# Kernel tuning notes

Hardware: AMD Instinct MI355X
Metric: run time of the kernel (lower is better)

The kernel has to match this reference:

```python
import jax, jax.numpy as jnp
import numpy as np

NUM_HEADS = 4
LOCAL_RADIUS = 2


def setup_inputs() -> dict:
    key = jax.random.key(0)
    ks = jax.random.split(key, 7)
    B, C, H, W = 1, 256, 40, 40
    O = 256  # out_channels
    s = 1.0 / np.sqrt(C).astype(np.float32)
    x = jax.random.normal(ks[0], (B, C, H, W), dtype=jnp.float32)
    Wq = jax.random.normal(ks[1], (C, O), dtype=jnp.float32) * s
    Wk = jax.random.normal(ks[2], (C, O), dtype=jnp.float32) * s
    Wv = jax.random.normal(ks[3], (C, O), dtype=jnp.float32) * s
    bq = jnp.zeros((O,), jnp.float32)
    bk = jnp.zeros((O,), jnp.float32)
    bv = jnp.zeros((O,), jnp.float32)
    return {"x": x, "Wq": Wq, "bq": bq, "Wk": Wk, "bk": bk, "Wv": Wv, "bv": bv}


def reference(x, Wq, bq, Wk, bk, Wv, bv):
    B, C, H, W = x.shape
    N = H * W
    O = Wq.shape[1]
    hd = O // NUM_HEADS
    # Faithful to torch: x.view(B, N, -1) is a raw row-major reshape of (B,C,H,W)
    xf = x.reshape(B, N, C)
    # projections -> (B, heads, N, head_dim)
    q = (xf @ Wq + bq).reshape(B, N, NUM_HEADS, hd).transpose(0, 2, 1, 3)
    k = (xf @ Wk + bk).reshape(B, N, NUM_HEADS, hd).transpose(0, 2, 1, 3)
    v = (xf @ Wv + bv).reshape(B, N, NUM_HEADS, hd).transpose(0, 2, 1, 3)
    scale = jnp.asarray(O, jnp.float32) ** 0.5
    acc = jnp.zeros_like(v)
    # 25 shifted full-attention passes; roll is over (heads, points) axes,
    # exactly matching torch key.roll(shifts=(h,w), dims=(-3,-2)).
    for h in range(-LOCAL_RADIUS, LOCAL_RADIUS + 1):
        for w in range(-LOCAL_RADIUS, LOCAL_RADIUS + 1):
            rk = jnp.roll(k, shift=(h, w), axis=(1, 2))
            scores = jnp.einsum('bhnd,bhmd->bhnm', q, rk) / scale  # (B,h,N,N)
            attn = jax.nn.softmax(scores, axis=-1)
            rv = jnp.roll(v, shift=(-h, -w), axis=(1, 2))
            acc = acc + jnp.einsum('bhnm,bhmd->bhnd', attn, rv)
    # (B, heads, N, hd) -> (B, N, O)
    return acc.transpose(0, 2, 1, 3).reshape(B, N, O)
```

## Files before the change

kernel.cpp:

```cpp
#include <hip/hip_runtime.h>
#include <hip/hip_bf16.h>
#include <stdint.h>

typedef __attribute__((ext_vector_type(8))) __bf16 bf16x8;
typedef __attribute__((ext_vector_type(4))) float f32x4;

#define N_PTS 1600
#define HD    64

#define OFF_XC   0u
#define OFF_WT   819200u
#define OFF_BIAS 1212416u
#define OFF_VHT  1213952u
#define OFF_QH   2033152u
#define OFF_KH   2852352u
#define OFF_KF   0u
#define OFF_OP   2852352u
#define OFF_LP   9405952u
#define OFF_VF   9610752u

__device__ __forceinline__ float bf2f(ushort h) {
  union { uint32_t u; float f; } v; v.u = ((uint32_t)h) << 16; return v.f;
}
__device__ __forceinline__ ushort f2bf(float f) {
  union { float f; uint32_t u; } v; v.f = f;
  uint32_t u = v.u;
  return (ushort)((u + 0x7FFFu + ((u >> 16) & 1u)) >> 16);
}
__device__ __forceinline__ uint32_t pk2(float a, float b) {
  union { __hip_bfloat162 h; uint32_t u; } cv;
  cv.h = __float22bfloat162_rn(make_float2(a, b));
  return cv.u;
}

__device__ __forceinline__ int detect_f32(const ushort* xu, int* shflag) {
  int t = threadIdx.x & 255;
  if (t == 0) *shflag = 0;
  __syncthreads();
  int local = 0;
#pragma unroll
  for (int i = 0; i < 4; ++i) {
    float v = bf2f(xu[(t * 4 + i) * 2]);
    if (!(fabsf(v) < 1e4f)) local = 1;
  }
  if (local) atomicOr(shflag, 1);
  __syncthreads();
  return *shflag;
}

__global__ void k_prep(const void* __restrict__ x, const void* __restrict__ Wq,
                       const void* __restrict__ bq, const void* __restrict__ Wk,
                       const void* __restrict__ bk, const void* __restrict__ Wv,
                       const void* __restrict__ bv, char* __restrict__ ws) {
  __shared__ int shflag;
  __shared__ ushort tileb[32][33];
  int isf32 = detect_f32((const ushort*)x, &shflag);
  int b = blockIdx.x, t = threadIdx.x;

  if (b < 400) {
    ushort4 o;
    if (isf32) {
      float4 f = ((const float4*)x)[b * 256 + t];
      o.x = f2bf(f.x); o.y = f2bf(f.y); o.z = f2bf(f.z); o.w = f2bf(f.w);
    } else {
      o = ((const ushort4*)x)[b * 256 + t];
    }
    ((ushort4*)(ws + OFF_XC))[b * 256 + t] = o;
  } else if (b < 592) {
    int w = b - 400, z = w >> 6, tile = w & 63;
    const void* W = (z == 0) ? Wq : ((z == 1) ? Wk : Wv);
    int o0 = (tile & 7) * 32, k0 = (tile >> 3) * 32;
    int tx = t & 31, ty = t >> 5;
#pragma unroll
    for (int i = 0; i < 32; i += 8) {
      int kk = (k0 + ty + i) * 256 + o0 + tx;
      tileb[ty + i][tx] = isf32 ? f2bf(((const float*)W)[kk]) : ((const ushort*)W)[kk];
    }
    __syncthreads();
    ushort* WT = (ushort*)(ws + OFF_WT) + z * 65536;
#pragma unroll
    for (int i = 0; i < 32; i += 8)
      WT[(o0 + ty + i) * 256 + k0 + tx] = tileb[tx][ty + i];
  } else {
    ushort* bb = (ushort*)(ws + OFF_BIAS);
#pragma unroll
    for (int z = 0; z < 3; ++z) {
      const void* B = (z == 0) ? bq : ((z == 1) ? bk : bv);
      bb[z * 256 + t] = isf32 ? f2bf(((const float*)B)[t]) : ((const ushort*)B)[t];
    }
  }
}

__launch_bounds__(256)
__global__ void k_proj(const ushort* __restrict__ X, const ushort* __restrict__ WT,
                       const ushort* __restrict__ bias3,
                       ushort* __restrict__ Qh, ushort* __restrict__ Kh, ushort* __restrict__ VhT) {
  int z = blockIdx.z;
  const ushort* WTz = WT + z * 65536;
  const ushort* bias = bias3 + z * 256;
  int n0 = blockIdx.x * 16;
  int head = threadIdx.x >> 6;
  int lane = threadIdx.x & 63;
  int c = lane & 15, quad = lane >> 4;

  f32x4 acc[4];
#pragma unroll
  for (int i = 0; i < 4; ++i) acc[i] = (f32x4){0.f, 0.f, 0.f, 0.f};

  const ushort* xrow = X + (n0 + c) * 256;
#pragma unroll
  for (int kt = 0; kt < 8; ++kt) {
    bf16x8 a = *(const bf16x8*)(xrow + kt * 32 + quad * 8);
#pragma unroll
    for (int os = 0; os < 4; ++os) {
      bf16x8 bfr = *(const bf16x8*)(WTz + (head * 64 + os * 16 + c) * 256 + kt * 32 + quad * 8);
      acc[os] = __builtin_amdgcn_mfma_f32_16x16x32_bf16(a, bfr, acc[os], 0, 0, 0);
    }
  }
  if (z == 2) {
#pragma unroll
    for (int os = 0; os < 4; ++os) {
      float bval = bf2f(bias[head * 64 + os * 16 + c]);
      ushort4 v;
      v.x = f2bf(acc[os][0] + bval); v.y = f2bf(acc[os][1] + bval);
      v.z = f2bf(acc[os][2] + bval); v.w = f2bf(acc[os][3] + bval);
      *(ushort4*)(VhT + (head * 64 + os * 16 + c) * N_PTS + n0 + quad * 4) = v;
    }
  } else {
    float scale = (z == 0) ? 0.0625f * 1.44269504088896f : 1.0f;
    ushort* out = (z == 0) ? Qh : Kh;
#pragma unroll
    for (int os = 0; os < 4; ++os) {
      float bval = bf2f(bias[head * 64 + os * 16 + c]);
#pragma unroll
      for (int r = 0; r < 4; ++r)
        out[head * (N_PTS * HD) + (n0 + quad * 4 + r) * HD + os * 16 + c] =
            f2bf((acc[os][r] + bval) * scale);
    }
  }
}

__global__ void k_frag(const ushort* __restrict__ Kh, const ushort* __restrict__ VhT,
                       ushort* __restrict__ Kf, ushort* __restrict__ Vf) {
  int q = blockIdx.x * 256 + threadIdx.x;
  int isV = q >= 51200;
  int idx = isV ? q - 51200 : q;
  int lane = idx & 63, ch = (idx >> 6) & 3;
  int rest = idx >> 8;
  int t = rest % 50, g = rest / 50;
  int c = lane & 15, quad = lane >> 4;
  if (!isV) {
    int perm = ((c >> 2) << 3) + (c & 3);
    int key = t * 32 + perm + ((ch >> 1) << 2);
    int d0 = (ch & 1) * 32 + quad * 8;
    bf16x8 v = *(const bf16x8*)(Kh + (size_t)(g * N_PTS + key) * HD + d0);
    *(bf16x8*)(Kf + (size_t)idx * 8) = v;
  } else {
    int d = ch * 16 + c;
    int m0 = t * 32 + quad * 8;
    const ushort* row = VhT + (size_t)(g * HD + d) * N_PTS;
    int mp = (m0 == 0) ? 1592 : m0 - 8;
    int mn = (m0 == 1592) ? 0 : m0 + 8;
    union { bf16x8 v[3]; ushort us[24]; } w;
    w.v[0] = *(const bf16x8*)(row + mp);
    w.v[1] = *(const bf16x8*)(row + m0);
    w.v[2] = *(const bf16x8*)(row + mn);
    union { ushort us[8]; bf16x8 v; } o;
#pragma unroll
    for (int j = 0; j < 8; ++j) {
      float s = bf2f(w.us[4 + j]) + bf2f(w.us[6 + j]) + bf2f(w.us[8 + j]) +
                bf2f(w.us[10 + j]) + bf2f(w.us[12 + j]);
      o.us[j] = f2bf(s);
    }
    *(bf16x8*)(Vf + (size_t)idx * 8) = o.v;
  }
}

__device__ __forceinline__ bf16x8 pack_p8(const f32x4& s0, const f32x4& s1, float& lp) {
  float e0 = exp2f(s0[0]), e1 = exp2f(s0[1]), e2 = exp2f(s0[2]), e3 = exp2f(s0[3]);
  float e4 = exp2f(s1[0]), e5 = exp2f(s1[1]), e6 = exp2f(s1[2]), e7 = exp2f(s1[3]);
  lp += ((e0 + e1) + (e2 + e3)) + ((e4 + e5) + (e6 + e7));
  union { uint32_t u[4]; bf16x8 v; } r;
  r.u[0] = pk2(e0, e1); r.u[1] = pk2(e2, e3);
  r.u[2] = pk2(e4, e5); r.u[3] = pk2(e6, e7);
  return r.v;
}

#define MFMA16(a, b, cc) __builtin_amdgcn_mfma_f32_16x16x32_bf16(a, b, cc, 0, 0, 0)

#define LOADT(sfx, t) do {                                            \
    const char* kt_ = kfp + (size_t)(t) * 4096;                       \
    const char* vt_ = vfp + (size_t)(t) * 4096;                       \
    ka0##sfx = *(const bf16x8*)(kt_);                                 \
    ka1##sfx = *(const bf16x8*)(kt_ + 1024);                          \
    kb0##sfx = *(const bf16x8*)(kt_ + 2048);                          \
    kb1##sfx = *(const bf16x8*)(kt_ + 3072);                          \
    vb0##sfx = *(const bf16x8*)(vt_);                                 \
    vb1##sfx = *(const bf16x8*)(vt_ + 1024);                          \
    vb2##sfx = *(const bf16x8*)(vt_ + 2048);                          \
    vb3##sfx = *(const bf16x8*)(vt_ + 3072);                          \
  } while (0)

#define COMPUTE(sfx) do {                                             \
    __builtin_amdgcn_s_setprio(1);                                    \
    f32x4 s0 = MFMA16(ka0##sfx, qa00, z4);                            \
    s0 = MFMA16(ka1##sfx, qa01, s0);                                  \
    f32x4 s1 = MFMA16(kb0##sfx, qa00, z4);                            \
    s1 = MFMA16(kb1##sfx, qa01, s1);                                  \
    bf16x8 pa0 = pack_p8(s0, s1, lp0);                                \
    oacc0[0] = MFMA16(pa0, vb0##sfx, oacc0[0]);                       \
    oacc0[1] = MFMA16(pa0, vb1##sfx, oacc0[1]);                       \
    oacc0[2] = MFMA16(pa0, vb2##sfx, oacc0[2]);                       \
    oacc0[3] = MFMA16(pa0, vb3##sfx, oacc0[3]);                       \
    s0 = MFMA16(ka0##sfx, qa10, z4);                                  \
    s0 = MFMA16(ka1##sfx, qa11, s0);                                  \
    s1 = MFMA16(kb0##sfx, qa10, z4);                                  \
    s1 = MFMA16(kb1##sfx, qa11, s1);                                  \
    bf16x8 pa1 = pack_p8(s0, s1, lp1);                                \
    oacc1[0] = MFMA16(pa1, vb0##sfx, oacc1[0]);                       \
    oacc1[1] = MFMA16(pa1, vb1##sfx, oacc1[1]);                       \
    oacc1[2] = MFMA16(pa1, vb2##sfx, oacc1[2]);                       \
    oacc1[3] = MFMA16(pa1, vb3##sfx, oacc1[3]);                       \
    __builtin_amdgcn_s_setprio(0);                                    \
  } while (0)

__launch_bounds__(256)
__global__ void k_attn(const ushort* __restrict__ Qh, const ushort* __restrict__ Kf,
                       const ushort* __restrict__ Vf, ushort* __restrict__ Opart,
                       float* __restrict__ Lpart) {
  int qt = blockIdx.x;
  int yy = blockIdx.y;
  int hp = yy >> 2, kg = yy & 3;
  int vg = (2 * hp - kg + 8) & 3;
  int tid = threadIdx.x, sp = tid >> 6, lane = tid & 63;
  int c = lane & 15, quad = lane >> 4;
  int n0 = qt * 16;

  __shared__ float obuf[4][16][68];
  __shared__ float lbuf[4][16];

  const ushort* q0row = Qh + ((hp    ) * N_PTS + n0 + c) * HD;
  const ushort* q1row = Qh + ((hp + 2) * N_PTS + n0 + c) * HD;
  bf16x8 qa00 = *(const bf16x8*)(q0row + quad * 8);
  bf16x8 qa01 = *(const bf16x8*)(q0row + 32 + quad * 8);
  bf16x8 qa10 = *(const bf16x8*)(q1row + quad * 8);
  bf16x8 qa11 = *(const bf16x8*)(q1row + 32 + quad * 8);

  f32x4 oacc0[4], oacc1[4];
#pragma unroll
  for (int i = 0; i < 4; ++i) {
    oacc0[i] = (f32x4){0.f, 0.f, 0.f, 0.f};
    oacc1[i] = (f32x4){0.f, 0.f, 0.f, 0.f};
  }
  float lp0 = 0.f, lp1 = 0.f;

  int off = (sp == 0) ? 0 : (sp == 1) ? 13 : (sp == 2) ? 26 : 38;
  int iters = (sp < 2) ? 13 : 12;
  const f32x4 z4 = (f32x4){0.f, 0.f, 0.f, 0.f};

  const char* kfp = (const char*)Kf + (size_t)(kg * 50 + off) * 4096 + lane * 16;
  const char* vfp = (const char*)Vf + (size_t)(vg * 50 + off) * 4096 + lane * 16;

  bf16x8 ka0A, ka1A, kb0A, kb1A, vb0A, vb1A, vb2A, vb3A;
  bf16x8 ka0B, ka1B, kb0B, kb1B, vb0B, vb1B, vb2B, vb3B;

  LOADT(A, 0);
  int it = 0;
  for (; it + 2 <= iters; it += 2) {
    LOADT(B, it + 1);
    COMPUTE(A);
    int tn = (it + 2 < iters) ? (it + 2) : (it + 1);
    LOADT(A, tn);
    COMPUTE(B);
  }
  if (it < iters) COMPUTE(A);

  lp0 += __shfl_xor(lp0, 16, 64); lp0 += __shfl_xor(lp0, 32, 64);
  lp1 += __shfl_xor(lp1, 16, 64); lp1 += __shfl_xor(lp1, 32, 64);

#pragma unroll
  for (int h = 0; h < 2; ++h) {
    __syncthreads();
    const f32x4* oa = h ? oacc1 : oacc0;
#pragma unroll
    for (int ds = 0; ds < 4; ++ds)
#pragma unroll
      for (int r = 0; r < 4; ++r)
        obuf[sp][quad * 4 + r][ds * 16 + c] = oa[ds][r];
    if (quad == 0) lbuf[sp][c] = h ? lp1 : lp0;
    __syncthreads();

    int q = tid >> 4, d0 = (tid & 15) * 4;
    f32x4 a = *(const f32x4*)&obuf[0][q][d0];
    a += *(const f32x4*)&obuf[1][q][d0];
    a += *(const f32x4*)&obuf[2][q][d0];
    a += *(const f32x4*)&obuf[3][q][d0];
    float l = lbuf[0][q] + lbuf[1][q] + lbuf[2][q] + lbuf[3][q];
    int hq = hp + 2 * h;
    union { uint32_t u[2]; } wv;
    wv.u[0] = pk2(a[0], a[1]);
    wv.u[1] = pk2(a[2], a[3]);
    *(uint2*)&Opart[(size_t)(kg * N_PTS + n0 + q) * 256 + hq * 64 + d0] =
        *(uint2*)wv.u;
    if ((tid & 15) == 0)
      Lpart[(kg * 4 + hq) * N_PTS + n0 + q] = l;
  }
}

__global__ void k_out(const ushort* __restrict__ Opart, const float* __restrict__ Lpart,
                      const void* __restrict__ x, void* __restrict__ out) {
  __shared__ int shflag;
  int isf32 = detect_f32((const ushort*)x, &shflag);
  int idx = blockIdx.x * 256 + threadIdx.x;
  int n = idx >> 8, o = idx & 255, hq = o >> 6;
  float acc = 0.f;
#pragma unroll
  for (int kg = 0; kg < 4; ++kg) {
    float num = bf2f(Opart[(size_t)(kg * N_PTS + n) * 256 + o]);
    float l = Lpart[(kg * 4 + hq) * N_PTS + n];
    float w = (kg == ((hq + 2) & 3)) ? 2.f : 1.f;
    acc += w * num / l;
  }
  if (isf32) ((float*)out)[idx] = acc;
  else       ((ushort*)out)[idx] = f2bf(acc);
}

extern "C" void kernel_launch(void* const* d_in, const int* in_sizes, int n_in,
                              void* d_out, int out_size, void* d_ws, size_t ws_size,
                              hipStream_t stream) {
  char* ws = (char*)d_ws;
  ushort* Xc    = (ushort*)(ws + OFF_XC);
  ushort* WT    = (ushort*)(ws + OFF_WT);
  ushort* bias3 = (ushort*)(ws + OFF_BIAS);
  ushort* VhT   = (ushort*)(ws + OFF_VHT);
  ushort* Qh    = (ushort*)(ws + OFF_QH);
  ushort* Kh    = (ushort*)(ws + OFF_KH);
  ushort* Kf    = (ushort*)(ws + OFF_KF);
  ushort* Vf    = (ushort*)(ws + OFF_VF);
  ushort* Opart = (ushort*)(ws + OFF_OP);
  float*  Lpart = (float*)(ws + OFF_LP);

  k_prep<<<593, 256, 0, stream>>>(d_in[0], d_in[1], d_in[2], d_in[3],
                                  d_in[4], d_in[5], d_in[6], ws);
  k_proj<<<dim3(100, 1, 3), 256, 0, stream>>>(Xc, WT, bias3, Qh, Kh, VhT);
  k_frag<<<400, 256, 0, stream>>>(Kh, VhT, Kf, Vf);
  k_attn<<<dim3(100, 8), 256, 0, stream>>>(Qh, Kf, Vf, Opart, Lpart);
  k_out<<<1600, 256, 0, stream>>>(Opart, Lpart, d_in[0], d_out);
}
```

Before: 116.6 us.

## Fuse x conversion into projection and output combine into attention kernel

Drops the separate x-to-bf16 staging pass from the prep kernel and converts fp32 x on the fly inside the projection kernel. Restructures the attention launch so each 512-thread block handles all four key groups for a head pair across eight waves, two per group, splitting the sequence in halves. The normalization and weighted combine are then done in shared memory and written straight to the output, which removes the separate output kernel and its partial-result round trip through global memory. In exchange there are fewer attention blocks (200 instead of 800), so fewer blocks are in flight, and each block uses more shared memory.

Result: faster. 109.4 us (-6.2%).

```diff
diff --git a/kernel.cpp b/kernel.cpp
--- a/kernel.cpp
+++ b/kernel.cpp
@@ -8,16 +8,13 @@
 #define N_PTS 1600
 #define HD    64
 
-#define OFF_XC   0u
-#define OFF_WT   819200u
-#define OFF_BIAS 1212416u
-#define OFF_VHT  1213952u
-#define OFF_QH   2033152u
-#define OFF_KH   2852352u
-#define OFF_KF   0u
-#define OFF_OP   2852352u
-#define OFF_LP   9405952u
-#define OFF_VF   9610752u
+#define OFF_WT   0u
+#define OFF_BIAS 393216u
+#define OFF_VHT  394752u
+#define OFF_QH   1213952u
+#define OFF_KH   2033152u
+#define OFF_KF   2852352u
+#define OFF_VF   3671552u
 
 __device__ __forceinline__ float bf2f(ushort h) {
   union { uint32_t u; float f; } v; v.u = ((uint32_t)h) << 16; return v.f;
@@ -57,17 +54,8 @@
   int isf32 = detect_f32((const ushort*)x, &shflag);
   int b = blockIdx.x, t = threadIdx.x;
 
-  if (b < 400) {
-    ushort4 o;
-    if (isf32) {
-      float4 f = ((const float4*)x)[b * 256 + t];
-      o.x = f2bf(f.x); o.y = f2bf(f.y); o.z = f2bf(f.z); o.w = f2bf(f.w);
-    } else {
-      o = ((const ushort4*)x)[b * 256 + t];
-    }
-    ((ushort4*)(ws + OFF_XC))[b * 256 + t] = o;
-  } else if (b < 592) {
-    int w = b - 400, z = w >> 6, tile = w & 63;
+  if (b < 192) {
+    int z = b >> 6, tile = b & 63;
     const void* W = (z == 0) ? Wq : ((z == 1) ? Wk : Wv);
     int o0 = (tile & 7) * 32, k0 = (tile >> 3) * 32;
     int tx = t & 31, ty = t >> 5;
@@ -92,9 +80,11 @@
 }
 
 __launch_bounds__(256)
-__global__ void k_proj(const ushort* __restrict__ X, const ushort* __restrict__ WT,
+__global__ void k_proj(const void* __restrict__ x, const ushort* __restrict__ WT,
                        const ushort* __restrict__ bias3,
                        ushort* __restrict__ Qh, ushort* __restrict__ Kh, ushort* __restrict__ VhT) {
+  __shared__ int shflag;
+  int isf32 = detect_f32((const ushort*)x, &shflag);
   int z = blockIdx.z;
   const ushort* WTz = WT + z * 65536;
   const ushort* bias = bias3 + z * 256;
@@ -107,10 +97,23 @@
 #pragma unroll
   for (int i = 0; i < 4; ++i) acc[i] = (f32x4){0.f, 0.f, 0.f, 0.f};
 
-  const ushort* xrow = X + (n0 + c) * 256;
+  int ebase = (n0 + c) * 256;
 #pragma unroll
   for (int kt = 0; kt < 8; ++kt) {
-    bf16x8 a = *(const bf16x8*)(xrow + kt * 32 + quad * 8);
+    bf16x8 a;
+    if (isf32) {
+      const float4* X4 = (const float4*)x;
+      int i4 = (ebase + kt * 32 + quad * 8) >> 2;
+      float4 f0 = X4[i4], f1 = X4[i4 + 1];
+      union { ushort us[8]; bf16x8 v; } cv;
+      cv.us[0] = f2bf(f0.x); cv.us[1] = f2bf(f0.y);
+      cv.us[2] = f2bf(f0.z); cv.us[3] = f2bf(f0.w);
+      cv.us[4] = f2bf(f1.x); cv.us[5] = f2bf(f1.y);
+      cv.us[6] = f2bf(f1.z); cv.us[7] = f2bf(f1.w);
+      a = cv.v;
+    } else {
+      a = *(const bf16x8*)((const ushort*)x + ebase + kt * 32 + quad * 8);
+    }
 #pragma unroll
     for (int os = 0; os < 4; ++os) {
       bf16x8 bfr = *(const bf16x8*)(WTz + (head * 64 + os * 16 + c) * 256 + kt * 32 + quad * 8);
@@ -224,20 +227,22 @@
     __builtin_amdgcn_s_setprio(0);                                    \
   } while (0)
 
-__launch_bounds__(256)
+__launch_bounds__(512)
 __global__ void k_attn(const ushort* __restrict__ Qh, const ushort* __restrict__ Kf,
-                       const ushort* __restrict__ Vf, ushort* __restrict__ Opart,
-                       float* __restrict__ Lpart) {
+                       const ushort* __restrict__ Vf, const void* __restrict__ x,
+                       void* __restrict__ out) {
+  __shared__ int shflag;
+  __shared__ float obuf[8][16][68];
+  __shared__ float lbuf[8][16];
+  int isf32 = detect_f32((const ushort*)x, &shflag);
+
   int qt = blockIdx.x;
-  int yy = blockIdx.y;
-  int hp = yy >> 2, kg = yy & 3;
+  int hp = blockIdx.y;
+  int tid = threadIdx.x, sp = tid >> 6, lane = tid & 63;
+  int kg = sp & 3, zh = sp >> 2;
   int vg = (2 * hp - kg + 8) & 3;
-  int tid = threadIdx.x, sp = tid >> 6, lane = tid & 63;
   int c = lane & 15, quad = lane >> 4;
   int n0 = qt * 16;
-
-  __shared__ float obuf[4][16][68];
-  __shared__ float lbuf[4][16];
 
   const ushort* q0row = Qh + ((hp    ) * N_PTS + n0 + c) * HD;
   const ushort* q1row = Qh + ((hp + 2) * N_PTS + n0 + c) * HD;
@@ -254,8 +259,8 @@
   }
   float lp0 = 0.f, lp1 = 0.f;
 
-  int off = (sp == 0) ? 0 : (sp == 1) ? 13 : (sp == 2) ? 26 : 38;
-  int iters = (sp < 2) ? 13 : 12;
+  int off = zh * 25;
+  const int iters = 25;
   const f32x4 z4 = (f32x4){0.f, 0.f, 0.f, 0.f};
 
   const char* kfp = (const char*)Kf + (size_t)(kg * 50 + off) * 4096 + lane * 16;
@@ -290,46 +295,31 @@
     if (quad == 0) lbuf[sp][c] = h ? lp1 : lp0;
     __syncthreads();
 
-    int q = tid >> 4, d0 = (tid & 15) * 4;
-    f32x4 a = *(const f32x4*)&obuf[0][q][d0];
-    a += *(const f32x4*)&obuf[1][q][d0];
-    a += *(const f32x4*)&obuf[2][q][d0];
-    a += *(const f32x4*)&obuf[3][q][d0];
-    float l = lbuf[0][q] + lbuf[1][q] + lbuf[2][q] + lbuf[3][q];
+    int q = tid >> 5, dp = (tid & 31) * 2;
     int hq = hp + 2 * h;
-    union { uint32_t u[2]; } wv;
-    wv.u[0] = pk2(a[0], a[1]);
-    wv.u[1] = pk2(a[2], a[3]);
-    *(uint2*)&Opart[(size_t)(kg * N_PTS + n0 + q) * 256 + hq * 64 + d0] =
-        *(uint2*)wv.u;
-    if ((tid & 15) == 0)
-      Lpart[(kg * 4 + hq) * N_PTS + n0 + q] = l;
-  }
-}
-
-__global__ void k_out(const ushort* __restrict__ Opart, const float* __restrict__ Lpart,
-                      const void* __restrict__ x, void* __restrict__ out) {
-  __shared__ int shflag;
-  int isf32 = detect_f32((const ushort*)x, &shflag);
-  int idx = blockIdx.x * 256 + threadIdx.x;
-  int n = idx >> 8, o = idx & 255, hq = o >> 6;
-  float acc = 0.f;
-#pragma unroll
-  for (int kg = 0; kg < 4; ++kg) {
-    float num = bf2f(Opart[(size_t)(kg * N_PTS + n) * 256 + o]);
-    float l = Lpart[(kg * 4 + hq) * N_PTS + n];
-    float w = (kg == ((hq + 2) & 3)) ? 2.f : 1.f;
-    acc += w * num / l;
-  }
-  if (isf32) ((float*)out)[idx] = acc;
-  else       ((ushort*)out)[idx] = f2bf(acc);
+    float a0 = 0.f, a1 = 0.f;
+#pragma unroll
+    for (int g = 0; g < 4; ++g) {
+      float n0v = obuf[g][q][dp]     + obuf[g + 4][q][dp];
+      float n1v = obuf[g][q][dp + 1] + obuf[g + 4][q][dp + 1];
+      float l   = lbuf[g][q] + lbuf[g + 4][q];
+      float w   = (g == ((hq + 2) & 3)) ? 2.f : 1.f;
+      float rl  = w / l;
+      a0 += n0v * rl; a1 += n1v * rl;
+    }
+    size_t oidx = (size_t)(n0 + q) * 256 + hq * 64 + dp;
+    if (isf32) {
+      ((float2*)out)[oidx >> 1] = make_float2(a0, a1);
+    } else {
+      ((uint32_t*)out)[oidx >> 1] = pk2(a0, a1);
+    }
+  }
 }
 
 extern "C" void kernel_launch(void* const* d_in, const int* in_sizes, int n_in,
                               void* d_out, int out_size, void* d_ws, size_t ws_size,
                               hipStream_t stream) {
   char* ws = (char*)d_ws;
-  ushort* Xc    = (ushort*)(ws + OFF_XC);
   ushort* WT    = (ushort*)(ws + OFF_WT);
   ushort* bias3 = (ushort*)(ws + OFF_BIAS);
   ushort* VhT   = (ushort*)(ws + OFF_VHT);
@@ -337,13 +327,10 @@
   ushort* Kh    = (ushort*)(ws + OFF_KH);
   ushort* Kf    = (ushort*)(ws + OFF_KF);
   ushort* Vf    = (ushort*)(ws + OFF_VF);
-  ushort* Opart = (ushort*)(ws + OFF_OP);
-  float*  Lpart = (float*)(ws + OFF_LP);
-
-  k_prep<<<593, 256, 0, stream>>>(d_in[0], d_in[1], d_in[2], d_in[3],
+
+  k_prep<<<193, 256, 0, stream>>>(d_in[0], d_in[1], d_in[2], d_in[3],
                                   d_in[4], d_in[5], d_in[6], ws);
-  k_proj<<<dim3(100, 1, 3), 256, 0, stream>>>(Xc, WT, bias3, Qh, Kh, VhT);
+  k_proj<<<dim3(100, 1, 3), 256, 0, stream>>>(d_in[0], WT, bias3, Qh, Kh, VhT);
   k_frag<<<400, 256, 0, stream>>>(Kh, VhT, Kf, Vf);
-  k_attn<<<dim3(100, 8), 256, 0, stream>>>(Qh, Kf, Vf, Opart, Lpart);
-  k_out<<<1600, 256, 0, stream>>>(Opart, Lpart, d_in[0], d_out);
-}
+  k_attn<<<dim3(100, 2), 512, 0, stream>>>(Qh, Kf, Vf, d_in[0], d_out);
+}
```
